# Kernel tuning notes

Hardware: AMD Instinct MI355X
Metric: run time of the kernel (lower is better)

Reference implementation:

```python
import jax, jax.numpy as jnp
import numpy as np

ATTACK_RATE = 0.03

def setup_inputs() -> dict:
    key = jax.random.key(0)
    rec_audio = jax.random.normal(key, (256, 131072), dtype=jnp.float32)
    return {"rec_audio": rec_audio}

def reference(rec_audio):
    B, N = rec_audio.shape
    k = int(ATTACK_RATE * N)  # number of samples zeroed per row (without replacement)
    # Gumbel-trick style: per-row uniform scores; top-k scores pick k distinct indices,
    # equivalent to np.random.choice(replace=False) per row, fully vectorized.
    u = jax.random.uniform(jax.random.key(42), (B, N), dtype=jnp.float32)
    _, idx = jax.lax.top_k(u, k)                  # [B, k] distinct indices per row
    rows = jnp.arange(B)[:, None]                 # [B, 1]
    mask = jnp.ones((B, N), dtype=rec_audio.dtype).at[rows, idx].set(0.0)
    return rec_audio * mask
```

## Files before the change

### kernel.cpp

```cpp
#include <hip/hip_runtime.h>
#include <stdint.h>

#define NROWS 256
#define NCOLS 131072
#define KSEL  3932
#define TPB   1024
#define VITERS (NCOLS / (TPB * 4))
#define TM    8106908u
#define MAXC  5120
#define SBINS 256
#define MAXB  256

__device__ __forceinline__ uint32_t rotl32(uint32_t v, int r) {
    return __builtin_amdgcn_alignbit(v, v, 32 - r);
}

__device__ __forceinline__ uint32_t jax_bits(uint32_t j) {
    const uint32_t ks0 = 0u;
    const uint32_t ks1 = 42u;
    const uint32_t ks2 = ks0 ^ ks1 ^ 0x1BD11BDAu;
    uint32_t x0 = 0u + ks0;
    uint32_t x1 = j + ks1;
#define TF_RND(r) { x0 += x1; x1 = rotl32(x1, r); x1 ^= x0; }
    TF_RND(13) TF_RND(15) TF_RND(26) TF_RND(6)
    x0 += ks1; x1 += ks2 + 1u;
    TF_RND(17) TF_RND(29) TF_RND(16) TF_RND(24)
    x0 += ks2; x1 += ks0 + 2u;
    TF_RND(13) TF_RND(15) TF_RND(26) TF_RND(6)
    x0 += ks0; x1 += ks1 + 3u;
    TF_RND(17) TF_RND(29) TF_RND(16) TF_RND(24)
    x0 += ks1; x1 += ks2 + 4u;
    TF_RND(13) TF_RND(15) TF_RND(26) TF_RND(6)
    x0 += ks2; x1 += ks0 + 5u;
#undef TF_RND
    return x0 ^ x1;
}

__global__ __launch_bounds__(TPB) void topk_mask_kernel(const float* __restrict__ in,
                                                        float* __restrict__ out) {
    __shared__ uint32_t cm[MAXC];
    __shared__ uint32_t cidx[MAXC];
    __shared__ uint32_t hist[SBINS];
    __shared__ uint32_t scanb[SBINS];
    __shared__ uint32_t bkeys[MAXB];
    __shared__ uint32_t s_ccount;
    __shared__ uint32_t s_bcnt;
    __shared__ uint32_t s_bstar;
    __shared__ uint32_t s_r;
    __shared__ uint32_t s_tkey;

    const uint32_t row  = blockIdx.x;
    const uint32_t tid  = threadIdx.x;
    const uint32_t base = row * (uint32_t)NCOLS;

    if (tid < SBINS) hist[tid] = 0u;
    if (tid == 0) { s_ccount = 0u; s_bcnt = 0u; }
    __syncthreads();

    const float4* in4  = (const float4*)(in + base);
    float4*       out4 = (float4*)(out + base);
    for (int it = 0; it < VITERS; ++it) {
        uint32_t vi = (uint32_t)it * TPB + tid;
        uint32_t c  = vi * 4u;
        uint32_t j  = base + c;
        float4 v = in4[vi];
        uint32_t m0 = jax_bits(j + 0u) >> 9;
        uint32_t m1 = jax_bits(j + 1u) >> 9;
        uint32_t m2 = jax_bits(j + 2u) >> 9;
        uint32_t m3 = jax_bits(j + 3u) >> 9;
        out4[vi] = v;
        if (m0 >= TM) { uint32_t p = atomicAdd(&s_ccount, 1u); if (p < MAXC) { cm[p] = m0 - TM; cidx[p] = c + 0u; } }
        if (m1 >= TM) { uint32_t p = atomicAdd(&s_ccount, 1u); if (p < MAXC) { cm[p] = m1 - TM; cidx[p] = c + 1u; } }
        if (m2 >= TM) { uint32_t p = atomicAdd(&s_ccount, 1u); if (p < MAXC) { cm[p] = m2 - TM; cidx[p] = c + 2u; } }
        if (m3 >= TM) { uint32_t p = atomicAdd(&s_ccount, 1u); if (p < MAXC) { cm[p] = m3 - TM; cidx[p] = c + 3u; } }
    }
    __syncthreads();

    uint32_t cc = s_ccount; if (cc > MAXC) cc = MAXC;

    for (uint32_t i = tid; i < cc; i += TPB) atomicAdd(&hist[cm[i] >> 11], 1u);
    __syncthreads();

    uint32_t h = 0, S = 0;
    if (tid < SBINS) { h = hist[tid]; scanb[tid] = h; }
    __syncthreads();
    S = h;
    for (uint32_t off = 1; off < SBINS; off <<= 1) {
        uint32_t v = 0;
        if (tid < SBINS && tid + off < SBINS) v = scanb[tid + off];
        __syncthreads();
        if (tid < SBINS) { S += v; scanb[tid] = S; }
        __syncthreads();
    }
    if (tid < SBINS) {
        uint32_t above = S - h;
        if (above < KSEL && S >= KSEL) {
            s_bstar = tid;
            s_r = KSEL - above;
        }
    }
    __syncthreads();

    const uint32_t bstar = s_bstar;
    const uint32_t r     = s_r;

    for (uint32_t i = tid; i < cc; i += TPB) {
        if ((cm[i] >> 11) == bstar) {
            uint32_t p = atomicAdd(&s_bcnt, 1u);
            if (p < MAXB) bkeys[p] = ((cm[i] & 2047u) << 17) | (131071u - cidx[i]);
        }
    }
    __syncthreads();

    uint32_t bc = s_bcnt; if (bc > MAXB) bc = MAXB;
    if (tid < bc) {
        uint32_t mykey = bkeys[tid];
        uint32_t rank = 0;
        for (uint32_t i = 0; i < bc; ++i) rank += (bkeys[i] > mykey) ? 1u : 0u;
        if (rank == r - 1) s_tkey = mykey;
    }
    __syncthreads();

    const uint32_t tkey = s_tkey;

    for (uint32_t i = tid; i < cc; i += TPB) {
        uint32_t bin = cm[i] >> 11;
        bool z = (bin > bstar);
        if (bin == bstar) {
            uint32_t key = ((cm[i] & 2047u) << 17) | (131071u - cidx[i]);
            z = (key >= tkey);
        }
        if (z) out[base + cidx[i]] = 0.0f;
    }
}

extern "C" void kernel_launch(void* const* d_in, const int* in_sizes, int n_in,
                              void* d_out, int out_size, void* d_ws, size_t ws_size,
                              hipStream_t stream) {
    const float* in = (const float*)d_in[0];
    float* out = (float*)d_out;
    hipLaunchKernelGGL(topk_mask_kernel, dim3(NROWS), dim3(TPB), 0, stream, in, out);
}
```

Before: 295.9 us.

## Split top-k mask into parallel half-row streaming pass and per-row select kernel

Splits the fused per-row kernel into a streaming pass that runs two blocks per row and appends candidate column indices to a global workspace with global atomics, plus a separate select kernel that recomputes the random keys for the candidates and finds the threshold. This doubles the number of blocks in the compute-heavy RNG pass to raise occupancy and CU utilisation. In exchange it adds two extra kernel launches, global atomic contention, and workspace traffic, and candidate order now depends on cross-block interleaving.

```diff
diff --git a/kernel.cpp b/kernel.cpp
--- a/kernel.cpp
+++ b/kernel.cpp
@@ -5,8 +5,10 @@
 #define NCOLS 131072
 #define KSEL  3932
 #define TPB   1024
-#define VITERS (NCOLS / (TPB * 4))
+#define HALF  (NCOLS / 2)
+#define H_ITERS (HALF / (TPB * 4))
 #define TM    8106908u
+#define TB    (TM << 9)
 #define MAXC  5120
 #define SBINS 256
 #define MAXB  256
@@ -36,14 +38,51 @@
     return x0 ^ x1;
 }
 
-__global__ __launch_bounds__(TPB) void topk_mask_kernel(const float* __restrict__ in,
-                                                        float* __restrict__ out) {
+__global__ void zero_counts(uint32_t* __restrict__ cnt) {
+    cnt[threadIdx.x] = 0u;
+}
+
+__global__ __launch_bounds__(TPB, 8) void pass1_kernel(const float* __restrict__ in,
+                                                       float* __restrict__ out,
+                                                       uint32_t* __restrict__ cnt,
+                                                       uint32_t* __restrict__ cidx_g) {
+    const uint32_t bid  = blockIdx.x;
+    const uint32_t row  = bid >> 1;
+    const uint32_t half = bid & 1u;
+    const uint32_t tid  = threadIdx.x;
+    const uint32_t hbase = row * (uint32_t)NCOLS + half * (uint32_t)HALF;
+
+    const float4* in4  = (const float4*)(in + hbase);
+    float4*       out4 = (float4*)(out + hbase);
+    uint32_t* myidx = cidx_g + row * (uint32_t)MAXC;
+    uint32_t* mycnt = cnt + row;
+    const uint32_t colbase = half * (uint32_t)HALF;
+
+    for (int it = 0; it < H_ITERS; ++it) {
+        uint32_t vi = (uint32_t)it * TPB + tid;
+        uint32_t c  = vi * 4u;
+        uint32_t j  = hbase + c;
+        float4 v = in4[vi];
+        uint32_t b0 = jax_bits(j + 0u);
+        uint32_t b1 = jax_bits(j + 1u);
+        uint32_t b2 = jax_bits(j + 2u);
+        uint32_t b3 = jax_bits(j + 3u);
+        out4[vi] = v;
+        if (b0 >= TB) { uint32_t p = atomicAdd(mycnt, 1u); if (p < MAXC) myidx[p] = colbase + c + 0u; }
+        if (b1 >= TB) { uint32_t p = atomicAdd(mycnt, 1u); if (p < MAXC) myidx[p] = colbase + c + 1u; }
+        if (b2 >= TB) { uint32_t p = atomicAdd(mycnt, 1u); if (p < MAXC) myidx[p] = colbase + c + 2u; }
+        if (b3 >= TB) { uint32_t p = atomicAdd(mycnt, 1u); if (p < MAXC) myidx[p] = colbase + c + 3u; }
+    }
+}
+
+__global__ __launch_bounds__(TPB) void select_kernel(float* __restrict__ out,
+                                                     const uint32_t* __restrict__ cnt,
+                                                     const uint32_t* __restrict__ cidx_g) {
     __shared__ uint32_t cm[MAXC];
     __shared__ uint32_t cidx[MAXC];
     __shared__ uint32_t hist[SBINS];
     __shared__ uint32_t scanb[SBINS];
     __shared__ uint32_t bkeys[MAXB];
-    __shared__ uint32_t s_ccount;
     __shared__ uint32_t s_bcnt;
     __shared__ uint32_t s_bstar;
     __shared__ uint32_t s_r;
@@ -54,31 +93,19 @@
     const uint32_t base = row * (uint32_t)NCOLS;
 
     if (tid < SBINS) hist[tid] = 0u;
-    if (tid == 0) { s_ccount = 0u; s_bcnt = 0u; }
+    if (tid == 0) s_bcnt = 0u;
     __syncthreads();
 
-    const float4* in4  = (const float4*)(in + base);
-    float4*       out4 = (float4*)(out + base);
-    for (int it = 0; it < VITERS; ++it) {
-        uint32_t vi = (uint32_t)it * TPB + tid;
-        uint32_t c  = vi * 4u;
-        uint32_t j  = base + c;
-        float4 v = in4[vi];
-        uint32_t m0 = jax_bits(j + 0u) >> 9;
-        uint32_t m1 = jax_bits(j + 1u) >> 9;
-        uint32_t m2 = jax_bits(j + 2u) >> 9;
-        uint32_t m3 = jax_bits(j + 3u) >> 9;
-        out4[vi] = v;
-        if (m0 >= TM) { uint32_t p = atomicAdd(&s_ccount, 1u); if (p < MAXC) { cm[p] = m0 - TM; cidx[p] = c + 0u; } }
-        if (m1 >= TM) { uint32_t p = atomicAdd(&s_ccount, 1u); if (p < MAXC) { cm[p] = m1 - TM; cidx[p] = c + 1u; } }
-        if (m2 >= TM) { uint32_t p = atomicAdd(&s_ccount, 1u); if (p < MAXC) { cm[p] = m2 - TM; cidx[p] = c + 2u; } }
-        if (m3 >= TM) { uint32_t p = atomicAdd(&s_ccount, 1u); if (p < MAXC) { cm[p] = m3 - TM; cidx[p] = c + 3u; } }
+    uint32_t cc = cnt[row]; if (cc > MAXC) cc = MAXC;
+
+    for (uint32_t i = tid; i < cc; i += TPB) {
+        uint32_t col = cidx_g[row * (uint32_t)MAXC + i];
+        uint32_t m = jax_bits(base + col) >> 9;
+        uint32_t d = m - TM;
+        cm[i] = d;
+        cidx[i] = col;
+        atomicAdd(&hist[d >> 11], 1u);
     }
-    __syncthreads();
-
-    uint32_t cc = s_ccount; if (cc > MAXC) cc = MAXC;
-
-    for (uint32_t i = tid; i < cc; i += TPB) atomicAdd(&hist[cm[i] >> 11], 1u);
     __syncthreads();
 
     uint32_t h = 0, S = 0;
@@ -139,5 +166,10 @@
                               hipStream_t stream) {
     const float* in = (const float*)d_in[0];
     float* out = (float*)d_out;
-    hipLaunchKernelGGL(topk_mask_kernel, dim3(NROWS), dim3(TPB), 0, stream, in, out);
+    uint32_t* cnt    = (uint32_t*)d_ws;
+    uint32_t* cidx_g = (uint32_t*)d_ws + NROWS;
+
+    hipLaunchKernelGGL(zero_counts, dim3(1), dim3(NROWS), 0, stream, cnt);
+    hipLaunchKernelGGL(pass1_kernel, dim3(NROWS * 2), dim3(TPB), 0, stream, in, out, cnt, cidx_g);
+    hipLaunchKernelGGL(select_kernel, dim3(NROWS), dim3(TPB), 0, stream, out, cnt, cidx_g);
 }
```

New measurement: 768.4 us. 2.6x slower.
